# Kernel tuning notes

Hardware: AMD Instinct MI355X
Metric: run time of the kernel (lower is better)

Reference implementation:

```python
import jax, jax.numpy as jnp
import numpy as np


def setup_inputs() -> dict:
    key = jax.random.key(0)
    x = jax.random.normal(key, (2, 64, 128), dtype=jnp.float32)
    return {"x": x}


def reference(x):
    # Faithful vectorization of the triple-permutation range-mean loop.
    # Original: for all permutations (lm, tr, sp) of range(L) (all distinct),
    #   dist[:, lm, tr, sp] = concat(mean(x[:, min(lm,sp):max(lm,sp)]),
    #                                 mean(x[:, min(tr,sp):max(tr,sp)]))
    # Non-permutation index triples (any two equal) remain zero.
    B, L, F = x.shape
    # Exclusive prefix sum: P[:, i] = sum_{j < i} x[:, j]  -> O(1) range sums
    P = jnp.concatenate([jnp.zeros((B, 1, F), x.dtype), jnp.cumsum(x, axis=1)], axis=1)  # [B, L+1, F]
    idx = jnp.arange(L)
    lo = jnp.minimum(idx[:, None], idx[None, :])  # [L, L]
    hi = jnp.maximum(idx[:, None], idx[None, :])  # [L, L]
    denom = jnp.maximum(hi - lo, 1).astype(x.dtype)  # avoid 0/0 on diagonal (masked out later)
    # M[b, a, c, f] = mean of x[b, min(a,c):max(a,c), f]
    M = (P[:, hi] - P[:, lo]) / denom[None, :, :, None]  # [B, L, L, F]

    first = jnp.broadcast_to(M[:, :, None, :, :], (B, L, L, L, F))   # indexed by (lm, sp), bcast over tr
    second = jnp.broadcast_to(M[:, None, :, :, :], (B, L, L, L, F))  # indexed by (tr, sp), bcast over lm

    lm = idx[:, None, None]
    tr = idx[None, :, None]
    sp = idx[None, None, :]
    distinct = ((lm != tr) & (lm != sp) & (tr != sp))  # [L, L, L]
    mask = distinct[None, :, :, :, None].astype(x.dtype)

    dist = jnp.concatenate([first, second], axis=-1) * mask  # [B, L, L, L, 2F]
    return dist
```

## Files before the change

### kernel.cpp

```cpp
#include <hip/hip_runtime.h>
#include <hip/hip_bf16.h>


#define B_ 2
#define L_ 64
#define F_ 128

typedef float f32x4 __attribute__((ext_vector_type(4)));

__device__ float g_P[B_ * (L_ + 1) * F_];

__global__ void prefix_kernel(const float* __restrict__ x) {
    const int b = blockIdx.x;
    const int f = threadIdx.x;
    const float* xb = x + b * L_ * F_ + f;
    float* Pb = g_P + b * (L_ + 1) * F_ + f;

    float v[L_];
#pragma unroll
    for (int r = 0; r < L_; ++r) v[r] = xb[r * F_];

    float run = 0.0f;
    Pb[0] = 0.0f;
#pragma unroll
    for (int r = 0; r < L_; ++r) {
        run += v[r];
        Pb[(r + 1) * F_] = run;
    }
}

__global__ __launch_bounds__(256) void writer_kernel(f32x4* __restrict__ out) {
    const int bid = blockIdx.x;
    const int tg = bid & 15;
    const int a  = (bid >> 4) & 63;
    const int b  = bid >> 10;
    const int t0 = tg << 2;
    const int tid = threadIdx.x;
    const int f4 = tid & 63;
    const int s0 = (tid >> 6) << 4;

    f32x4* o = out + ((size_t)(((b << 6) + a) << 6) + t0) * 4096 + s0 * 64 + f4;

    const f32x4 z = {0.f, 0.f, 0.f, 0.f};
    const bool lower = (f4 < 32);
    const float* base = g_P + ((b * (L_ + 1)) << 7) + ((f4 & 31) << 2);

    f32x4 p[16];
#pragma unroll
    for (int k = 0; k < 16; ++k)
        p[k] = *reinterpret_cast<const f32x4*>(base + ((s0 + k) << 7));
    const f32x4 pa = *reinterpret_cast<const f32x4*>(base + (a << 7));
    f32x4 pt[4];
#pragma unroll
    for (int tt = 0; tt < 4; ++tt)
        pt[tt] = *reinterpret_cast<const f32x4*>(base + ((t0 + tt) << 7));
    const float fa = (float)a;

#pragma unroll
    for (int tt = 0; tt < 4; ++tt) {
        const int t = t0 + tt;
        const bool plane_zero = (a == t);
        const f32x4 pi = lower ? pa : pt[tt];
        const float fi = lower ? fa : (float)t;
        f32x4* ot = o + tt * 4096;

#pragma unroll
        for (int k = 0; k < 16; ++k) {
            const int s = s0 + k;
            f32x4 v;
            if (plane_zero || s == a || s == t) {
                v = z;
            } else {
                const float r = __builtin_amdgcn_rcpf((float)s - fi);
                v = (p[k] - pi) * r;
            }
            ot[k * 64] = v;
        }
    }
}

extern "C" void kernel_launch(void* const* d_in, const int* in_sizes, int n_in,
                              void* d_out, int out_size, void* d_ws, size_t ws_size,
                              hipStream_t stream) {
    const float* x = (const float*)d_in[0];
    f32x4* out = (f32x4*)d_out;

    prefix_kernel<<<B_, F_, 0, stream>>>(x);
    writer_kernel<<<B_ * L_ * (L_ / 4), 256, 0, stream>>>(out);
}
```

Before: 102.0 us.

## Fuse prefix-sum into writer kernel and double tr planes per block

Removes the separate prefix kernel and its global scratch array. Each writer thread now recomputes the running prefix sum over all 64 rows of x, capturing the values it needs for s, t, and a. Blocks also cover 8 tr planes instead of 4, which halves the grid so the recomputation is amortised over more output. This drops one launch and a dependency between kernels, at the cost of redundant reads of x and more arithmetic and registers per thread.

```diff
diff --git a/kernel.cpp b/kernel.cpp
--- a/kernel.cpp
+++ b/kernel.cpp
@@ -8,56 +8,41 @@
 
 typedef float f32x4 __attribute__((ext_vector_type(4)));
 
-__device__ float g_P[B_ * (L_ + 1) * F_];
-
-__global__ void prefix_kernel(const float* __restrict__ x) {
-    const int b = blockIdx.x;
-    const int f = threadIdx.x;
-    const float* xb = x + b * L_ * F_ + f;
-    float* Pb = g_P + b * (L_ + 1) * F_ + f;
-
-    float v[L_];
-#pragma unroll
-    for (int r = 0; r < L_; ++r) v[r] = xb[r * F_];
-
-    float run = 0.0f;
-    Pb[0] = 0.0f;
-#pragma unroll
-    for (int r = 0; r < L_; ++r) {
-        run += v[r];
-        Pb[(r + 1) * F_] = run;
-    }
-}
-
-__global__ __launch_bounds__(256) void writer_kernel(f32x4* __restrict__ out) {
+__global__ __launch_bounds__(256) void writer_kernel(f32x4* __restrict__ out,
+                                                     const float* __restrict__ x) {
     const int bid = blockIdx.x;
-    const int tg = bid & 15;
-    const int a  = (bid >> 4) & 63;
-    const int b  = bid >> 10;
-    const int t0 = tg << 2;
+    const int tg = bid & 7;
+    const int a  = (bid >> 3) & 63;
+    const int b  = bid >> 9;
+    const int t0 = tg << 3;
     const int tid = threadIdx.x;
     const int f4 = tid & 63;
-    const int s0 = (tid >> 6) << 4;
+    const int sw = tid >> 6;
+    const int s0 = sw << 4;
 
     f32x4* o = out + ((size_t)(((b << 6) + a) << 6) + t0) * 4096 + s0 * 64 + f4;
 
-    const f32x4 z = {0.f, 0.f, 0.f, 0.f};
     const bool lower = (f4 < 32);
-    const float* base = g_P + ((b * (L_ + 1)) << 7) + ((f4 & 31) << 2);
+    const int c = (f4 & 31) << 2;
+    const float* xb = x + (b << 13) + c;
 
     f32x4 p[16];
+    f32x4 pt[8];
+    f32x4 pa  = {0.f, 0.f, 0.f, 0.f};
+    f32x4 run = {0.f, 0.f, 0.f, 0.f};
 #pragma unroll
-    for (int k = 0; k < 16; ++k)
-        p[k] = *reinterpret_cast<const f32x4*>(base + ((s0 + k) << 7));
-    const f32x4 pa = *reinterpret_cast<const f32x4*>(base + (a << 7));
-    f32x4 pt[4];
-#pragma unroll
-    for (int tt = 0; tt < 4; ++tt)
-        pt[tt] = *reinterpret_cast<const f32x4*>(base + ((t0 + tt) << 7));
+    for (int r = 0; r < L_; ++r) {
+        if ((r >> 4) == sw) p[r & 15] = run;
+        if ((r >> 3) == tg) pt[r & 7] = run;
+        if (r == a)         pa        = run;
+        run += *reinterpret_cast<const f32x4*>(xb + (r << 7));
+    }
+
+    const f32x4 z = {0.f, 0.f, 0.f, 0.f};
     const float fa = (float)a;
 
 #pragma unroll
-    for (int tt = 0; tt < 4; ++tt) {
+    for (int tt = 0; tt < 8; ++tt) {
         const int t = t0 + tt;
         const bool plane_zero = (a == t);
         const f32x4 pi = lower ? pa : pt[tt];
@@ -85,6 +70,5 @@
     const float* x = (const float*)d_in[0];
     f32x4* out = (f32x4*)d_out;
 
-    prefix_kernel<<<B_, F_, 0, stream>>>(x);
-    writer_kernel<<<B_ * L_ * (L_ / 4), 256, 0, stream>>>(out);
+    writer_kernel<<<B_ * L_ * (L_ / 8), 256, 0, stream>>>(out, x);
 }
```

Measured after the change: 159.4 us. +56.3%, slower.
